# Performance work log

Measured on AMD Instinct MI355X. Metric: run time of the kernel, lower is better.

The kernel has to match this reference:

```python
import jax, jax.numpy as jnp
import numpy as np

N_HEADS = 4

def layernorm(x, g, b):
    m = jnp.mean(x, -1, keepdims=True)
    v = jnp.var(x, -1, keepdims=True)
    return (x - m) / jnp.sqrt(v + 1e-5) * g + b

def conv1d(x, w, b, pad):
    y = jax.lax.conv_general_dilated(x, w, (1,), [(pad, pad)], dimension_numbers=('NCH', 'OIH', 'NCH'))
    return y + b[None, :, None]

def bn_eval(x, g, b, m, v):
    return (x - m[None, :, None]) / jnp.sqrt(v[None, :, None] + 1e-5) * g[None, :, None] + b[None, :, None]

def maxpool(x, k):
    return jax.lax.reduce_window(x, -jnp.inf, jax.lax.max, (1, 1, k), (1, 1, k), 'VALID')

def _forward(x, conv1_w, conv1_b, bn1_g, bn1_b, bn1_m, bn1_v, conv2_w, conv2_b, bn2_g, bn2_b, bn2_m, bn2_v, adj_prior, log_weights, gat_n1_g, gat_n1_b, gat_qkv_w, gat_qkv_b, gat_out_w, gat_out_b, gat_n2_g, gat_n2_b, gat_f1_w, gat_f1_b, gat_f2_w, gat_f2_b, gatn_g, gatn_b, gru_wih, gru_whh, gru_bih, gru_bhh, gate_w, gate_b):
    B, C, T = x.shape
    D = conv2_w.shape[0]
    dk = D // N_HEADS
    scale = dk ** -0.5
    # --- per-channel temporal CNN: (B,C,T) -> (B,C,T',D), T' = T//16 ---
    h = x.reshape(B * C, 1, T)
    h = maxpool(jax.nn.gelu(bn_eval(conv1d(h, conv1_w, conv1_b, 3), bn1_g, bn1_b, bn1_m, bn1_v), approximate=False), 4)
    h = maxpool(jax.nn.gelu(bn_eval(conv1d(h, conv2_w, conv2_b, 2), bn2_g, bn2_b, bn2_m, bn2_v), approximate=False), 4)
    Tp = h.shape[-1]
    h = jnp.transpose(h, (0, 2, 1)).reshape(B, C, Tp, D)
    # --- spectral dynamic adjacency ---
    h_avg = h.mean(axis=2)                                   # (B,C,D)
    hc = h_avg - h_avg.mean(-1, keepdims=True)
    hn = hc / (jnp.linalg.norm(hc, axis=-1, keepdims=True) + 1e-8)
    feat_corr = jnp.einsum('bcd,bed->bce', hn, hn)
    Xp = jnp.abs(jnp.fft.rfft(x, axis=-1))
    Xn = Xp / (jnp.linalg.norm(Xp, axis=-1, keepdims=True) + 1e-8)
    spec_coh = jnp.einsum('bcf,bef->bce', Xn, Xn)
    prior = (adj_prior + adj_prior.T)[None]
    w = jax.nn.softmax(log_weights)
    adj = w[0] * feat_corr + w[1] * spec_coh + w[2] * prior  # (B,C,C)
    # --- GAT stack over the C-node channel graph at every timestep ---
    ht = jnp.transpose(h, (0, 2, 1, 3)).reshape(B * Tp, C, D)
    adj_t = jnp.broadcast_to(adj[:, None], (B, Tp, C, C)).reshape(B * Tp, C, C)
    L = gat_qkv_w.shape[0]
    for l in range(L):
        hn1 = layernorm(ht, gat_n1_g[l], gat_n1_b[l])
        qkv = (hn1 @ gat_qkv_w[l].T + gat_qkv_b[l]).reshape(B * Tp, C, 3, N_HEADS, dk)
        q = jnp.moveaxis(qkv[:, :, 0], 1, 2)                 # (N,H,C,dk)
        k = jnp.moveaxis(qkv[:, :, 1], 1, 2)
        v = jnp.moveaxis(qkv[:, :, 2], 1, 2)
        attn = jnp.einsum('nhqd,nhkd->nhqk', q, k) * scale + adj_t[:, None]
        attn = jax.nn.softmax(attn, axis=-1)                 # dropout off (eval)
        out = jnp.einsum('nhqk,nhkd->nhqd', attn, v)
        out = jnp.moveaxis(out, 1, 2).reshape(B * Tp, C, D)
        ht = ht + out @ gat_out_w[l].T + gat_out_b[l]
        hn2 = layernorm(ht, gat_n2_g[l], gat_n2_b[l])
        ffn = jax.nn.gelu(hn2 @ gat_f1_w[l].T + gat_f1_b[l], approximate=False) @ gat_f2_w[l].T + gat_f2_b[l]
        ht = ht + ffn
    ht = layernorm(ht, gatn_g, gatn_b)
    hs = ht.reshape(B, Tp, C, D).transpose(0, 2, 1, 3).reshape(B * C, Tp, D)
    # --- bidirectional GRU (1 layer), final hidden states only ---
    G = gru_whh.shape[-1]
    def gru_last(xs, wih, whh, bih, bhh):
        def step(hprev, xt):
            gi = xt @ wih.T + bih
            gh = hprev @ whh.T + bhh
            ir, iz, inn = jnp.split(gi, 3, -1)
            hr, hz, hnn = jnp.split(gh, 3, -1)
            r = jax.nn.sigmoid(ir + hr)
            z = jax.nn.sigmoid(iz + hz)
            n = jnp.tanh(inn + r * hnn)
            hnew = (1.0 - z) * n + z * hprev
            return hnew, None
        h0 = jnp.zeros((xs.shape[0], G), xs.dtype)
        hl, _ = jax.lax.scan(step, h0, jnp.moveaxis(xs, 1, 0))
        return hl
    h_f = gru_last(hs, gru_wih[0], gru_whh[0], gru_bih[0], gru_bhh[0])
    h_b = gru_last(hs[:, ::-1], gru_wih[1], gru_whh[1], gru_bih[1], gru_bhh[1])
    h_out = jnp.concatenate([h_f, h_b], -1).reshape(B, C, 2 * G)
    # --- channel-attention readout ---
    gate = jax.nn.sigmoid(h_out @ gate_w.T + gate_b)         # (B,C,1)
    readout = (h_out * gate).sum(1) / (gate.sum(1) + 1e-8)   # (B,2G)
    return readout, adj, gate

def setup_inputs() -> dict:
    key = jax.random.key(0)
    ks = iter(jax.random.split(key, 64))
    B, C, T = 32, 16, 4096
    D, L, G = 64, 2, 64
    def rn(shape, s=0.08):
        return jax.random.normal(next(ks), shape, jnp.float32) * s
    return dict(
        x=jax.random.normal(next(ks), (B, C, T), jnp.float32),
        conv1_w=rn((32, 1, 7), 0.2), conv1_b=rn((32,)),
        bn1_g=jnp.ones((32,)), bn1_b=jnp.zeros((32,)), bn1_m=jnp.zeros((32,)), bn1_v=jnp.ones((32,)),
        conv2_w=rn((D, 32, 5), 0.1), conv2_b=rn((D,)),
        bn2_g=jnp.ones((D,)), bn2_b=jnp.zeros((D,)), bn2_m=jnp.zeros((D,)), bn2_v=jnp.ones((D,)),
        adj_prior=rn((C, C), 0.1), log_weights=jnp.zeros((3,)),
        gat_n1_g=jnp.ones((L, D)), gat_n1_b=jnp.zeros((L, D)),
        gat_qkv_w=rn((L, 3 * D, D)), gat_qkv_b=jnp.zeros((L, 3 * D)),
        gat_out_w=rn((L, D, D)), gat_out_b=jnp.zeros((L, D)),
        gat_n2_g=jnp.ones((L, D)), gat_n2_b=jnp.zeros((L, D)),
        gat_f1_w=rn((L, 2 * D, D)), gat_f1_b=jnp.zeros((L, 2 * D)),
        gat_f2_w=rn((L, D, 2 * D)), gat_f2_b=jnp.zeros((L, D)),
        gatn_g=jnp.ones((D,)), gatn_b=jnp.zeros((D,)),
        gru_wih=rn((2, 3 * G, D)), gru_whh=rn((2, 3 * G, G)),
        gru_bih=jnp.zeros((2, 3 * G)), gru_bhh=jnp.zeros((2, 3 * G)),
        gate_w=rn((1, 2 * G)), gate_b=jnp.zeros((1,)),
    )

def reference(x, conv1_w, conv1_b, bn1_g, bn1_b, bn1_m, bn1_v, conv2_w, conv2_b, bn2_g, bn2_b, bn2_m, bn2_v, adj_prior, log_weights, gat_n1_g, gat_n1_b, gat_qkv_w, gat_qkv_b, gat_out_w, gat_out_b, gat_n2_g, gat_n2_b, gat_f1_w, gat_f1_b, gat_f2_w, gat_f2_b, gatn_g, gatn_b, gru_wih, gru_whh, gru_bih, gru_bhh, gate_w, gate_b):
    return _forward(x, conv1_w, conv1_b, bn1_g, bn1_b, bn1_m, bn1_v, conv2_w, conv2_b, bn2_g, bn2_b, bn2_m, bn2_v, adj_prior, log_weights, gat_n1_g, gat_n1_b, gat_qkv_w, gat_qkv_b, gat_out_w, gat_out_b, gat_n2_g, gat_n2_b, gat_f1_w, gat_f1_b, gat_f2_w, gat_f2_b, gatn_g, gatn_b, gru_wih, gru_whh, gru_bih, gru_bhh, gate_w, gate_b)
```

## Files before the change

### kernel.cpp

```cpp
#include <hip/hip_runtime.h>
#include <hip/hip_bf16.h>
#include <math.h>

typedef __hip_bfloat16 bf16;
typedef unsigned short ushort_t;
typedef __attribute__((ext_vector_type(8))) short short8;
typedef __attribute__((ext_vector_type(4))) float f32x4;

__device__ __forceinline__ float b2f(bf16 v) { return __bfloat162float(v); }
__device__ __forceinline__ bf16 f2b(float v) { return __float2bfloat16(v); }
__device__ __forceinline__ float bflo(unsigned u) { return __uint_as_float(u << 16); }
__device__ __forceinline__ float bfhi(unsigned u) { return __uint_as_float(u & 0xffff0000u); }
__device__ __forceinline__ float sigmoidf_(float x) { return 1.0f / (1.0f + __expf(-x)); }

__device__ __forceinline__ float geluf(float x) {
    float z = x * 0.70710678118654752f;
    float az = fabsf(z);
    float t = 1.0f / (1.0f + 0.3275911f * az);
    float poly = ((((1.061405429f * t - 1.453152027f) * t + 1.421413741f) * t
                   - 0.284496736f) * t + 0.254829592f) * t;
    float erfa = 1.0f - poly * __expf(-z * z);
    float er = (z < 0.f) ? -erfa : erfa;
    return 0.5f * x * (1.0f + er);
}

__device__ __forceinline__ unsigned pack2bf(float a, float b) {
    unsigned ua = __float_as_uint(a); ua = (ua + 0x7FFFu + ((ua >> 16) & 1u)) >> 16;
    unsigned ub = __float_as_uint(b); ub = (ub + 0x7FFFu + ((ub >> 16) & 1u)) >> 16;
    return ua | (ub << 16);
}
__device__ __forceinline__ ushort_t f2bu(float v) {
    unsigned u = __float_as_uint(v);
    u = (u + 0x7FFFu + ((u >> 16) & 1u)) >> 16;
    return (ushort_t)u;
}

__global__ __launch_bounds__(256) void k_detect(const unsigned* __restrict__ x, int* __restrict__ flag)
{
    __shared__ int cnt;
    if (threadIdx.x == 0) cnt = 0;
    __syncthreads();
    unsigned u = x[threadIdx.x] & 0xFFFFu;
    float f = __uint_as_float(u << 16);
    float a = fabsf(f);
    int sane = (f == 0.0f) || (a > 1e-8f && a < 1e4f);
    atomicAdd(&cnt, sane);
    __syncthreads();
    if (threadIdx.x == 0) *flag = (cnt >= 160) ? 1 : 0;
}

struct InPtrs { const void* p[35]; };
struct InOffs { int off[35]; int sz[35]; };

__global__ __launch_bounds__(256) void k_convert(InPtrs P, InOffs O, int total,
                                                 const int* __restrict__ flag,
                                                 float* __restrict__ cvt)
{
    int idx = blockIdx.x * 256 + threadIdx.x;
    if (idx >= total) return;
    int isb = *flag;
    float v = 0.f;
#pragma unroll 1
    for (int s = 0; s < 35; s++) {
        int rel = idx - O.off[s];
        if (rel >= 0 && rel < O.sz[s]) {
            v = isb ? b2f(((const bf16*)P.p[s])[rel]) : ((const float*)P.p[s])[rel];
            break;
        }
    }
    cvt[idx] = v;
}

__global__ __launch_bounds__(256) void k_pack(const float* __restrict__ qw, const float* __restrict__ ow,
                                              const float* __restrict__ f1w, const float* __restrict__ f2w,
                                              const float* __restrict__ gwih, const float* __restrict__ gwhh,
                                              const float* __restrict__ c2w,
                                              unsigned* __restrict__ dst)
{
    int i = blockIdx.x * 256 + threadIdx.x;
    if (i >= 62464) return;
    if (i >= 57344) {
        int j0 = (i - 57344) * 2;
        int tap = j0 >> 11, rem = j0 & 2047;
        int d = rem >> 5, ic = rem & 31;
        dst[i] = pack2bf(c2w[d * 160 + ic * 5 + tap], c2w[d * 160 + (ic + 1) * 5 + tap]);
        return;
    }
    const float* s; int rel;
    if (i < 12288)      { s = qw;   rel = i; }
    else if (i < 16384) { s = ow;   rel = i - 12288; }
    else if (i < 24576) { s = f1w;  rel = i - 16384; }
    else if (i < 32768) { s = f2w;  rel = i - 24576; }
    else if (i < 45056) { s = gwih; rel = i - 32768; }
    else                { s = gwhh; rel = i - 45056; }
    dst[i] = pack2bf(s[2 * rel], s[2 * rel + 1]);
}

__global__ __launch_bounds__(256) void k_cnn(
    const float* __restrict__ x, const float* __restrict__ c1w, const float* __restrict__ c1b,
    const float* __restrict__ bn1g, const float* __restrict__ bn1b, const float* __restrict__ bn1m, const float* __restrict__ bn1v,
    const float* __restrict__ c2b,
    const float* __restrict__ bn2g, const float* __restrict__ bn2b, const float* __restrict__ bn2m, const float* __restrict__ bn2v,
    const ushort_t* __restrict__ w2pk,
    float* __restrict__ h_main)
{
    __shared__ float ubuf[4352];
    __shared__ ushort_t h1t[260 * 40];
    __shared__ float A2s[64], B2s[64];
    int bc = blockIdx.x, t = threadIdx.x;
    int l = t & 63, w = t >> 6;
    int lo = l & 15, quad = l >> 4;

    if (t < 64) {
        float s = bn2g[t] * rsqrtf(bn2v[t] + 1e-5f);
        A2s[t] = s; B2s[t] = (c2b[t] - bn2m[t]) * s + bn2b[t];
    }
    int icp = t & 15;
    float w1r[2][7], A1r[2], B1r[2];
#pragma unroll
    for (int s = 0; s < 2; s++) {
        int ic = icp * 2 + s;
#pragma unroll
        for (int k = 0; k < 7; k++) w1r[s][k] = c1w[ic * 7 + k];
        float sc = bn1g[ic] * rsqrtf(bn1v[ic] + 1e-5f);
        A1r[s] = sc; B1r[s] = (c1b[ic] - bn1m[ic]) * sc + bn1b[ic];
    }
    short8 Afr[4][5];
#pragma unroll
    for (int dt = 0; dt < 4; dt++)
#pragma unroll
        for (int tap = 0; tap < 5; tap++)
            Afr[dt][tap] = *(const short8*)(w2pk + ((tap * 64 + dt * 16 + lo) * 32 + quad * 8));

    const float* xrow = x + (size_t)bc * 4096;
    for (int tile = 0; tile < 4; tile++) {
        int X0 = 1024 * tile - 11;
        for (int i = t; i < 1056; i += 256) {
            int g = X0 + i;
            ubuf[i] = (g >= 0 && g < 4096) ? xrow[g] : 0.0f;
        }
        __syncthreads();
        for (int pos = (t >> 4); pos < 260; pos += 16) {
            const float4* xw = (const float4*)&ubuf[4 * pos];
            float4 fa = xw[0], fb = xw[1], fc = xw[2];
            float xv[12] = {fa.x, fa.y, fa.z, fa.w, fb.x, fb.y, fb.z, fb.w,
                            fc.x, fc.y, fc.z, fc.w};
            int t1pg = tile * 256 + pos - 2;
            bool ok = (t1pg >= 0 && t1pg < 1024);
            float res[2];
#pragma unroll
            for (int s = 0; s < 2; s++) {
                float a0 = 0.f, a1 = 0.f, a2 = 0.f, a3 = 0.f;
#pragma unroll
                for (int k = 0; k < 7; k++) {
                    float wv = w1r[s][k];
                    a0 += xv[k] * wv;     a1 += xv[k + 1] * wv;
                    a2 += xv[k + 2] * wv; a3 += xv[k + 3] * wv;
                }
                float A = A1r[s], B = B1r[s];
                a0 = a0 * A + B; a1 = a1 * A + B; a2 = a2 * A + B; a3 = a3 * A + B;
                float mx = fmaxf(fmaxf(a0, a1), fmaxf(a2, a3));
                float mn = fminf(fminf(a0, a1), fminf(a2, a3));
                res[s] = ok ? fmaxf(geluf(mx), geluf(mn)) : 0.0f;
            }
            ((unsigned*)h1t)[pos * 20 + icp] = pack2bf(res[0], res[1]);
        }
        __syncthreads();
        float* houtile = ubuf;
#pragma unroll
        for (int ni = 0; ni < 4; ni++) {
            int nt = w * 4 + ni;
            short8 bf[5];
#pragma unroll
            for (int tap = 0; tap < 5; tap++)
                bf[tap] = *(const short8*)&h1t[(nt * 16 + lo + tap) * 40 + quad * 8];
#pragma unroll
            for (int dt = 0; dt < 4; dt++) {
                f32x4 acc = {0.f, 0.f, 0.f, 0.f};
#pragma unroll
                for (int tap = 0; tap < 5; tap++)
                    acc = __builtin_amdgcn_mfma_f32_16x16x32_bf16(Afr[dt][tap], bf[tap], acc, 0, 0, 0);
                const float4 a2 = *(const float4*)&A2s[dt * 16 + quad * 4];
                const float4 b2 = *(const float4*)&B2s[dt * 16 + quad * 4];
                float a2a[4] = {a2.x, a2.y, a2.z, a2.w};
                float b2a[4] = {b2.x, b2.y, b2.z, b2.w};
#pragma unroll
                for (int r = 0; r < 4; r++) {
                    float v = acc[r] * a2a[r] + b2a[r];
                    float o1 = __shfl_xor(v, 1);
                    float mx = fmaxf(v, o1), mn = fminf(v, o1);
                    float mx2 = __shfl_xor(mx, 2), mn2 = __shfl_xor(mn, 2);
                    mx = fmaxf(mx, mx2); mn = fminf(mn, mn2);
                    float res = fmaxf(geluf(mx), geluf(mn));
                    if ((lo & 3) == 0)
                        houtile[(nt * 4 + (lo >> 2)) * 68 + dt * 16 + quad * 4 + r] = res;
                }
            }
        }
        __syncthreads();
        float* dst = h_main + (size_t)bc * 16384 + tile * 4096;
        for (int i = t * 4; i < 4096; i += 1024) {
            float4 v = *(const float4*)&ubuf[(i >> 6) * 68 + (i & 63)];
            *(float4*)&dst[i] = v;
        }
        __syncthreads();
    }
}

__global__ __launch_bounds__(512) void k_fft(const float* __restrict__ x, float* __restrict__ Xn)
{
    __shared__ float re[4096];
    __shared__ float im[4096];
    __shared__ float red[8];
    int bc = blockIdx.x, t = threadIdx.x;
    const float* xr = x + (size_t)bc * 4096;
    for (int i = t; i < 4096; i += 512) {
        int r = __brev((unsigned)i) >> 20;
        re[r] = xr[i];
        im[r] = 0.f;
    }
    __syncthreads();
    for (int s = 1; s <= 12; s++) {
        int half = 1 << (s - 1);
        float ang = -6.283185307179586f / (float)(1 << s);
        for (int m = t; m < 2048; m += 512) {
            int j = m & (half - 1);
            int pos = ((m >> (s - 1)) << s) | j;
            float sn, cs;
            __sincosf(ang * (float)j, &sn, &cs);
            float ur = re[pos], ui = im[pos];
            float vr = re[pos + half], vi = im[pos + half];
            float tr = vr * cs - vi * sn;
            float ti = vr * sn + vi * cs;
            re[pos] = ur + tr; im[pos] = ui + ti;
            re[pos + half] = ur - tr; im[pos + half] = ui - ti;
        }
        __syncthreads();
    }
    float mag[5];
    float ss = 0.f;
    int cnt = 0;
    for (int f = t; f <= 2048; f += 512) {
        float m2 = re[f] * re[f] + im[f] * im[f];
        mag[cnt++] = sqrtf(m2);
        ss += m2;
    }
    for (int off = 32; off; off >>= 1) ss += __shfl_xor(ss, off, 64);
    if ((t & 63) == 0) red[t >> 6] = ss;
    __syncthreads();
    float tot = 0.f;
#pragma unroll
    for (int i = 0; i < 8; i++) tot += red[i];
    float inv = 1.0f / (sqrtf(tot) + 1e-8f);
    cnt = 0;
    for (int f = t; f <= 2048; f += 512) Xn[(size_t)bc * 2049 + f] = mag[cnt++] * inv;
}

__global__ __launch_bounds__(64) void k_havg(const float* __restrict__ hm, float* __restrict__ hnf)
{
    int bc = blockIdx.x, d = threadIdx.x;
    const float* base = hm + (size_t)bc * 16384;
    float s = 0.f;
    for (int tp = 0; tp < 256; tp++) s += base[tp * 64 + d];
    float avg = s * (1.0f / 256.0f);
    float tot = avg;
    for (int off = 32; off; off >>= 1) tot += __shfl_xor(tot, off, 64);
    float hc = avg - tot * (1.0f / 64.0f);
    float sq = hc * hc;
    for (int off = 32; off; off >>= 1) sq += __shfl_xor(sq, off, 64);
    hnf[bc * 64 + d] = hc / (sqrtf(sq) + 1e-8f);
}

__global__ __launch_bounds__(256) void k_adj(
    const float* __restrict__ Xn, const float* __restrict__ hnf,
    const float* __restrict__ prior, const float* __restrict__ logw,
    float* __restrict__ adjw, void* __restrict__ out, const int* __restrict__ flag)
{
    __shared__ float xt[16][257];
    __shared__ float hh[16 * 64];
    int b = blockIdx.x, t = threadIdx.x;
    int c = t >> 4, e = t & 15;
    for (int i = t; i < 1024; i += 256) hh[i] = hnf[b * 1024 + i];
    __syncthreads();
    float fc = 0.f;
    for (int d = 0; d < 64; d++) fc += hh[c * 64 + d] * hh[e * 64 + d];
    float sc = 0.f;
    const float* Xb = Xn + (size_t)b * 16 * 2049;
    for (int f0 = 0; f0 < 2048; f0 += 256) {
        __syncthreads();
        for (int i = t; i < 16 * 256; i += 256) {
            int rr = i >> 8, ff = i & 255;
            xt[rr][ff] = Xb[rr * 2049 + f0 + ff];
        }
        __syncthreads();
        for (int ff = 0; ff < 256; ff++) sc += xt[c][ff] * xt[e][ff];
    }
    sc += Xb[c * 2049 + 2048] * Xb[e * 2049 + 2048];
    float l0 = logw[0], l1 = logw[1], l2 = logw[2];
    float mx = fmaxf(l0, fmaxf(l1, l2));
    float e0 = __expf(l0 - mx), e1 = __expf(l1 - mx), e2 = __expf(l2 - mx);
    float isum = 1.0f / (e0 + e1 + e2);
    float pr = prior[c * 16 + e] + prior[e * 16 + c];
    float v = (e0 * fc + e1 * sc + e2 * pr) * isum;
    adjw[b * 256 + t] = v;
    if (*flag) ((bf16*)out)[4096 + b * 256 + t] = f2b(v);
    else       ((float*)out)[4096 + b * 256 + t] = v;
}

__device__ __forceinline__ void ln_wave(const float (*ht)[68], ushort_t (*out)[72],
                                        const float* __restrict__ g, const float* __restrict__ bp,
                                        int quad, int lo)
{
    float v[16];
    const float4* row = (const float4*)(&ht[lo][quad * 16]);
#pragma unroll
    for (int i = 0; i < 4; i++) {
        float4 a = row[i];
        v[4 * i] = a.x; v[4 * i + 1] = a.y; v[4 * i + 2] = a.z; v[4 * i + 3] = a.w;
    }
    float s = 0.f;
#pragma unroll
    for (int i = 0; i < 16; i++) s += v[i];
    s += __shfl_xor(s, 16); s += __shfl_xor(s, 32);
    float mean = s * (1.0f / 64.0f);
    float q = 0.f;
#pragma unroll
    for (int i = 0; i < 16; i++) { float d = v[i] - mean; q += d * d; }
    q += __shfl_xor(q, 16); q += __shfl_xor(q, 32);
    float rstd = rsqrtf(q * (1.0f / 64.0f) + 1e-5f);
    const float4* gp = (const float4*)(g + quad * 16);
    const float4* bb4 = (const float4*)(bp + quad * 16);
    unsigned* orow = (unsigned*)(&out[lo][quad * 16]);
#pragma unroll
    for (int i = 0; i < 4; i++) {
        float4 gg = gp[i], bb = bb4[i];
        float o0 = (v[4 * i] - mean) * rstd * gg.x + bb.x;
        float o1 = (v[4 * i + 1] - mean) * rstd * gg.y + bb.y;
        float o2 = (v[4 * i + 2] - mean) * rstd * gg.z + bb.z;
        float o3 = (v[4 * i + 3] - mean) * rstd * gg.w + bb.w;
        orow[2 * i] = pack2bf(o0, o1);
        orow[2 * i + 1] = pack2bf(o2, o3);
    }
}

__global__ __launch_bounds__(256) void k_gat(
    const float* __restrict__ hm, const float* __restrict__ adjw,
    const ushort_t* __restrict__ wpk,
    const float* __restrict__ qb_, const float* __restrict__ ob_,
    const float* __restrict__ f1b_, const float* __restrict__ f2b_,
    const float* __restrict__ n1g_, const float* __restrict__ n1b_,
    const float* __restrict__ n2g_, const float* __restrict__ n2b_,
    const float* __restrict__ gng, const float* __restrict__ gnb,
    ushort_t* __restrict__ hmb)
{
    __shared__ float htw_all[4][16][68];
    __shared__ ushort_t hnw_all[4][16][72];
    __shared__ ushort_t qkb_all[4][16][200];
    __shared__ ushort_t pb_all[4][16][72];
    __shared__ ushort_t vt_all[4][64][24];
    int t = threadIdx.x;
    int w = t >> 6, l = t & 63;
    int quad = l >> 4, lo = l & 15;
    int n = blockIdx.x * 4 + w;
    int b = n >> 8, tp = n & 255;
    float (*htw)[68] = htw_all[w];
    ushort_t (*hnw)[72] = hnw_all[w];
    ushort_t (*qkb)[200] = qkb_all[w];
    ushort_t (*pb)[72] = pb_all[w];
    ushort_t (*vt)[24] = vt_all[w];
    const float* src = hm + (size_t)b * 16 * 16384 + (size_t)tp * 64;
#pragma unroll
    for (int c = 0; c < 16; c++) htw[c][l] = src[(size_t)c * 16384 + l];
    float adjr[4];
#pragma unroll
    for (int r = 0; r < 4; r++) adjr[r] = adjw[b * 256 + (quad * 4 + r) * 16 + lo];

    for (int layer = 0; layer < 2; layer++) {
        const ushort_t* wq  = wpk + layer * 12288;
        const ushort_t* wo  = wpk + 24576 + layer * 4096;
        const ushort_t* wf1 = wpk + 32768 + layer * 8192;
        const ushort_t* wf2 = wpk + 49152 + layer * 8192;
        const float* qb = qb_ + layer * 192;
        const float* ob = ob_ + layer * 64;
        const float* f1b = f1b_ + layer * 128;
        const float* f2b = f2b_ + layer * 64;

        ln_wave(htw, hnw, n1g_ + layer * 64, n1b_ + layer * 64, quad, lo);

        short8 a0 = *(const short8*)&hnw[lo][quad * 8];
        short8 a1 = *(const short8*)&hnw[lo][32 + quad * 8];
#pragma unroll
        for (int nt = 0; nt < 12; nt++) {
            const ushort_t* wr = wq + (nt * 16 + lo) * 64 + quad * 8;
            short8 b0 = *(const short8*)wr;
            short8 b1 = *(const short8*)(wr + 32);
            f32x4 acc = {0.f, 0.f, 0.f, 0.f};
            acc = __builtin_amdgcn_mfma_f32_16x16x32_bf16(a0, b0, acc, 0, 0, 0);
            acc = __builtin_amdgcn_mfma_f32_16x16x32_bf16(a1, b1, acc, 0, 0, 0);
            float bias = qb[nt * 16 + lo];
            if (nt < 8) {
#pragma unroll
                for (int r = 0; r < 4; r++) qkb[quad * 4 + r][nt * 16 + lo] = f2bu(acc[r] + bias);
            } else {
#pragma unroll
                for (int r = 0; r < 4; r++) vt[(nt - 8) * 16 + lo][quad * 4 + r] = f2bu(acc[r] + bias);
            }
        }

        short8 zf = {0, 0, 0, 0, 0, 0, 0, 0};
#pragma unroll
        for (int h = 0; h < 4; h++) {
            short8 qf = zf, kf = zf;
            if (quad < 2) {
                qf = *(const short8*)&qkb[lo][h * 16 + quad * 8];
                kf = *(const short8*)&qkb[lo][64 + h * 16 + quad * 8];
            }
            f32x4 s4 = {0.f, 0.f, 0.f, 0.f};
            s4 = __builtin_amdgcn_mfma_f32_16x16x32_bf16(qf, kf, s4, 0, 0, 0);
#pragma unroll
            for (int r = 0; r < 4; r++) {
                float sv = s4[r] * 0.25f + adjr[r];
                float mx = sv;
                mx = fmaxf(mx, __shfl_xor(mx, 1));
                mx = fmaxf(mx, __shfl_xor(mx, 2));
                mx = fmaxf(mx, __shfl_xor(mx, 4));
                mx = fmaxf(mx, __shfl_xor(mx, 8));
                float e = __expf(sv - mx);
                float sm = e;
                sm += __shfl_xor(sm, 1);
                sm += __shfl_xor(sm, 2);
                sm += __shfl_xor(sm, 4);
                sm += __shfl_xor(sm, 8);
                pb[quad * 4 + r][h * 16 + lo] = f2bu(e / sm);
            }
        }
#pragma unroll
        for (int h = 0; h < 4; h++) {
            short8 pf = zf, vf = zf;
            if (quad < 2) {
                pf = *(const short8*)&pb[lo][h * 16 + quad * 8];
                vf = *(const short8*)&vt[h * 16 + lo][quad * 8];
            }
            f32x4 oc = {0.f, 0.f, 0.f, 0.f};
            oc = __builtin_amdgcn_mfma_f32_16x16x32_bf16(pf, vf, oc, 0, 0, 0);
#pragma unroll
            for (int r = 0; r < 4; r++) qkb[quad * 4 + r][h * 16 + lo] = f2bu(oc[r]);
        }
        short8 pa0 = *(const short8*)&qkb[lo][quad * 8];
        short8 pa1 = *(const short8*)&qkb[lo][32 + quad * 8];
#pragma unroll
        for (int nt = 0; nt < 4; nt++) {
            const ushort_t* wr = wo + (nt * 16 + lo) * 64 + quad * 8;
            short8 b0 = *(const short8*)wr;
            short8 b1 = *(const short8*)(wr + 32);
            f32x4 acc = {0.f, 0.f, 0.f, 0.f};
            acc = __builtin_amdgcn_mfma_f32_16x16x32_bf16(pa0, b0, acc, 0, 0, 0);
            acc = __builtin_amdgcn_mfma_f32_16x16x32_bf16(pa1, b1, acc, 0, 0, 0);
            float bias = ob[nt * 16 + lo];
#pragma unroll
            for (int r = 0; r < 4; r++) htw[quad * 4 + r][nt * 16 + lo] += acc[r] + bias;
        }
        ln_wave(htw, hnw, n2g_ + layer * 64, n2b_ + layer * 64, quad, lo);
        short8 fa0 = *(const short8*)&hnw[lo][quad * 8];
        short8 fa1 = *(const short8*)&hnw[lo][32 + quad * 8];
#pragma unroll
        for (int nt = 0; nt < 8; nt++) {
            const ushort_t* wr = wf1 + (nt * 16 + lo) * 64 + quad * 8;
            short8 b0 = *(const short8*)wr;
            short8 b1 = *(const short8*)(wr + 32);
            f32x4 acc = {0.f, 0.f, 0.f, 0.f};
            acc = __builtin_amdgcn_mfma_f32_16x16x32_bf16(fa0, b0, acc, 0, 0, 0);
            acc = __builtin_amdgcn_mfma_f32_16x16x32_bf16(fa1, b1, acc, 0, 0, 0);
            float bias = f1b[nt * 16 + lo];
#pragma unroll
            for (int r = 0; r < 4; r++) qkb[quad * 4 + r][nt * 16 + lo] = f2bu(geluf(acc[r] + bias));
        }
        short8 ga[4];
#pragma unroll
        for (int kb = 0; kb < 4; kb++) ga[kb] = *(const short8*)&qkb[lo][kb * 32 + quad * 8];
#pragma unroll
        for (int nt = 0; nt < 4; nt++) {
            const ushort_t* wr = wf2 + (nt * 16 + lo) * 128 + quad * 8;
            f32x4 acc = {0.f, 0.f, 0.f, 0.f};
#pragma unroll
            for (int kb = 0; kb < 4; kb++) {
                short8 bb = *(const short8*)(wr + kb * 32);
                acc = __builtin_amdgcn_mfma_f32_16x16x32_bf16(ga[kb], bb, acc, 0, 0, 0);
            }
            float bias = f2b[nt * 16 + lo];
#pragma unroll
            for (int r = 0; r < 4; r++) htw[quad * 4 + r][nt * 16 + lo] += acc[r] + bias;
        }
    }
    {
        float v[16];
        const float4* row = (const float4*)(&htw[lo][quad * 16]);
#pragma unroll
        for (int i = 0; i < 4; i++) {
            float4 a = row[i];
            v[4 * i] = a.x; v[4 * i + 1] = a.y; v[4 * i + 2] = a.z; v[4 * i + 3] = a.w;
        }
        float s = 0.f;
#pragma unroll
        for (int i = 0; i < 16; i++) s += v[i];
        s += __shfl_xor(s, 16); s += __shfl_xor(s, 32);
        float mean = s * (1.0f / 64.0f);
        float q = 0.f;
#pragma unroll
        for (int i = 0; i < 16; i++) { float d = v[i] - mean; q += d * d; }
        q += __shfl_xor(q, 16); q += __shfl_xor(q, 32);
        float rstd = rsqrtf(q * (1.0f / 64.0f) + 1e-5f);
        const float4* gp = (const float4*)(gng + quad * 16);
        const float4* bb4 = (const float4*)(gnb + quad * 16);
        unsigned u[8];
#pragma unroll
        for (int i = 0; i < 4; i++) {
            float4 gg = gp[i], bb = bb4[i];
            float o0 = (v[4 * i] - mean) * rstd * gg.x + bb.x;
            float o1 = (v[4 * i + 1] - mean) * rstd * gg.y + bb.y;
            float o2 = (v[4 * i + 2] - mean) * rstd * gg.z + bb.z;
            float o3 = (v[4 * i + 3] - mean) * rstd * gg.w + bb.w;
            u[2 * i] = pack2bf(o0, o1);
            u[2 * i + 1] = pack2bf(o2, o3);
        }
        ushort_t* dst = hmb + (size_t)(b * 16 + lo) * 16384 + (size_t)tp * 64 + quad * 16;
        ((uint4*)dst)[0] = make_uint4(u[0], u[1], u[2], u[3]);
        ((uint4*)dst)[1] = make_uint4(u[4], u[5], u[6], u[7]);
    }
}

__global__ __launch_bounds__(256) void k_gru(
    const ushort_t* __restrict__ hmb, const ushort_t* __restrict__ wgru,
    const float* __restrict__ bih_, const float* __restrict__ bhh_,
    float* __restrict__ h_out)
{
    __shared__ ushort_t hbuf[2][16][72];
    int t = threadIdx.x;
    int w = t >> 6, l = t & 63;
    int ln = l & 15, qd = l >> 4;
    int dir = blockIdx.x >> 5;
    int cseq0 = (blockIdx.x & 31) * 16;
    const ushort_t* wih = wgru + dir * 12288;
    const ushort_t* whh = wgru + 24576 + dir * 12288;
    const ushort_t* pr0 = wih + ((w)*16 + ln) * 64 + qd * 8;
    const ushort_t* pz0 = wih + ((4 + w)*16 + ln) * 64 + qd * 8;
    const ushort_t* pn0 = wih + ((8 + w)*16 + ln) * 64 + qd * 8;
    const ushort_t* hr0 = whh + ((w)*16 + ln) * 64 + qd * 8;
    const ushort_t* hz0 = whh + ((4 + w)*16 + ln) * 64 + qd * 8;
    const ushort_t* hn0 = whh + ((8 + w)*16 + ln) * 64 + qd * 8;
    short8 wi_r0 = *(const short8*)pr0, wi_r1 = *(const short8*)(pr0 + 32);
    short8 wi_z0 = *(const short8*)pz0, wi_z1 = *(const short8*)(pz0 + 32);
    short8 wi_n0 = *(const short8*)pn0, wi_n1 = *(const short8*)(pn0 + 32);
    short8 wh_r0 = *(const short8*)hr0, wh_r1 = *(const short8*)(hr0 + 32);
    short8 wh_z0 = *(const short8*)hz0, wh_z1 = *(const short8*)(hz0 + 32);
    short8 wh_n0 = *(const short8*)hn0, wh_n1 = *(const short8*)(hn0 + 32);
    int d = w * 16 + ln;
    float bs_r = bih_[dir * 192 + d] + bhh_[dir * 192 + d];
    float bs_z = bih_[dir * 192 + 64 + d] + bhh_[dir * 192 + 64 + d];
    float bi_n = bih_[dir * 192 + 128 + d];
    float bh_n = bhh_[dir * 192 + 128 + d];
    const ushort_t* xrow = hmb + (size_t)(cseq0 + ln) * 16384 + qd * 8;
    for (int i = t; i < 2 * 16 * 72; i += 256) ((ushort_t*)hbuf)[i] = 0;
    float h_old[4] = {0.f, 0.f, 0.f, 0.f};
    int tt0 = dir ? 255 : 0;
    short8 xc0 = *(const short8*)(xrow + tt0 * 64);
    short8 xc1 = *(const short8*)(xrow + tt0 * 64 + 32);
    __syncthreads();
#pragma unroll 2
    for (int step = 0; step < 256; step++) {
        int cur = step & 1, nxt = cur ^ 1;
        short8 ah0 = *(const short8*)&hbuf[cur][ln][qd * 8];
        short8 ah1 = *(const short8*)&hbuf[cur][ln][32 + qd * 8];
        f32x4 ar = {0.f, 0.f, 0.f, 0.f}, az = {0.f, 0.f, 0.f, 0.f};
        f32x4 ani = {0.f, 0.f, 0.f, 0.f}, anh = {0.f, 0.f, 0.f, 0.f};
        ar = __builtin_amdgcn_mfma_f32_16x16x32_bf16(xc0, wi_r0, ar, 0, 0, 0);
        ar = __builtin_amdgcn_mfma_f32_16x16x32_bf16(xc1, wi_r1, ar, 0, 0, 0);
        ar = __builtin_amdgcn_mfma_f32_16x16x32_bf16(ah0, wh_r0, ar, 0, 0, 0);
        ar = __builtin_amdgcn_mfma_f32_16x16x32_bf16(ah1, wh_r1, ar, 0, 0, 0);
        az = __builtin_amdgcn_mfma_f32_16x16x32_bf16(xc0, wi_z0, az, 0, 0, 0);
        az = __builtin_amdgcn_mfma_f32_16x16x32_bf16(xc1, wi_z1, az, 0, 0, 0);
        az = __builtin_amdgcn_mfma_f32_16x16x32_bf16(ah0, wh_z0, az, 0, 0, 0);
        az = __builtin_amdgcn_mfma_f32_16x16x32_bf16(ah1, wh_z1, az, 0, 0, 0);
        ani = __builtin_amdgcn_mfma_f32_16x16x32_bf16(xc0, wi_n0, ani, 0, 0, 0);
        ani = __builtin_amdgcn_mfma_f32_16x16x32_bf16(xc1, wi_n1, ani, 0, 0, 0);
        anh = __builtin_amdgcn_mfma_f32_16x16x32_bf16(ah0, wh_n0, anh, 0, 0, 0);
        anh = __builtin_amdgcn_mfma_f32_16x16x32_bf16(ah1, wh_n1, anh, 0, 0, 0);
        if (step < 255) {
            int tn = dir ? (254 - step) : (step + 1);
            xc0 = *(const short8*)(xrow + tn * 64);
            xc1 = *(const short8*)(xrow + tn * 64 + 32);
        }
#pragma unroll
        for (int r = 0; r < 4; r++) {
            float gr = sigmoidf_(ar[r] + bs_r);
            float gz = sigmoidf_(az[r] + bs_z);
            float nin = (ani[r] + bi_n) + gr * (anh[r] + bh_n);
            nin = fminf(fmaxf(nin, -15.f), 15.f);
            float e = __expf(-2.f * nin);
            float gn = (1.f - e) / (1.f + e);
            float hn = gn + gz * (h_old[r] - gn);
            h_old[r] = hn;
            hbuf[nxt][qd * 4 + r][d] = f2bu(hn);
        }
        __syncthreads();
    }
#pragma unroll
    for (int r = 0; r < 4; r++)
        h_out[(size_t)(cseq0 + qd * 4 + r) * 128 + dir * 64 + d] = h_old[r];
}

__global__ __launch_bounds__(128) void k_readout(
    const float* __restrict__ h_out, const float* __restrict__ gw, const float* __restrict__ gb,
    void* __restrict__ out, const int* __restrict__ flag)
{
    __shared__ float gate_s[16];
    __shared__ float gws[128];
    int b = blockIdx.x, t = threadIdx.x;
    gws[t] = gw[t];
    __syncthreads();
    int isb = *flag;
    if (t < 16) {
        const float* hr = h_out + (size_t)(b * 16 + t) * 128;
        float acc = gb[0];
        for (int k = 0; k < 128; k++) acc += hr[k] * gws[k];
        float g = sigmoidf_(acc);
        gate_s[t] = g;
        if (isb) ((bf16*)out)[12288 + b * 16 + t] = f2b(g);
        else     ((float*)out)[12288 + b * 16 + t] = g;
    }
    __syncthreads();
    float den = 1e-8f;
#pragma unroll
    for (int c = 0; c < 16; c++) den += gate_s[c];
    float num = 0.f;
#pragma unroll
    for (int c = 0; c < 16; c++) num += h_out[(size_t)(b * 16 + c) * 128 + t] * gate_s[c];
    float v = num / den;
    if (isb) ((bf16*)out)[b * 128 + t] = f2b(v);
    else     ((float*)out)[b * 128 + t] = v;
}

extern "C" void kernel_launch(void* const* d_in, const int* in_sizes, int n_in,
                              void* d_out, int out_size, void* d_ws, size_t ws_size,
                              hipStream_t stream)
{
    int* flag = (int*)d_ws;
    float* cvt = (float*)((char*)d_ws + 256);

    InPtrs P;
    InOffs O;
    int cum = 0;
    for (int i = 0; i < 35; i++) {
        P.p[i] = d_in[i];
        O.off[i] = cum;
        O.sz[i] = in_sizes[i];
        cum += (in_sizes[i] + 7) & ~7;
    }
    int total = cum;

    const float* x     = cvt + O.off[0];
    const float* c1w   = cvt + O.off[1];
    const float* c1b   = cvt + O.off[2];
    const float* bn1g  = cvt + O.off[3];
    const float* bn1b  = cvt + O.off[4];
    const float* bn1m  = cvt + O.off[5];
    const float* bn1v  = cvt + O.off[6];
    const float* c2w   = cvt + O.off[7];
    const float* c2b   = cvt + O.off[8];
    const float* bn2g  = cvt + O.off[9];
    const float* bn2b  = cvt + O.off[10];
    const float* bn2m  = cvt + O.off[11];
    const float* bn2v  = cvt + O.off[12];
    const float* prior = cvt + O.off[13];
    const float* logw  = cvt + O.off[14];
    const float* n1g   = cvt + O.off[15];
    const float* n1b   = cvt + O.off[16];
    const float* qkvw  = cvt + O.off[17];
    const float* qkvb  = cvt + O.off[18];
    const float* outw  = cvt + O.off[19];
    const float* outb  = cvt + O.off[20];
    const float* n2g   = cvt + O.off[21];
    const float* n2b   = cvt + O.off[22];
    const float* f1w   = cvt + O.off[23];
    const float* f1b   = cvt + O.off[24];
    const float* f2w   = cvt + O.off[25];
    const float* f2b_  = cvt + O.off[26];
    const float* gng   = cvt + O.off[27];
    const float* gnb   = cvt + O.off[28];
    const float* gwih  = cvt + O.off[29];
    const float* gwhh  = cvt + O.off[30];
    const float* gbih  = cvt + O.off[31];
    const float* gbhh  = cvt + O.off[32];
    const float* gatew = cvt + O.off[33];
    const float* gateb = cvt + O.off[34];

    float* fbase = cvt + ((total + 63) & ~63);
    float* hm   = fbase;
    float* Xn   = hm + 8388608;
    float* hnf  = Xn + 1049088;
    float* adjw = hnf + 32768;
    float* hout = adjw + 8192;
    unsigned* wpk = (unsigned*)(hout + 65536);
    ushort_t* hmb = (ushort_t*)(wpk + 62464);

    k_detect<<<1, 256, 0, stream>>>((const unsigned*)d_in[0], flag);
    k_convert<<<(total + 255) / 256, 256, 0, stream>>>(P, O, total, flag, cvt);
    k_pack<<<244, 256, 0, stream>>>(qkvw, outw, f1w, f2w, gwih, gwhh, c2w, wpk);
    k_cnn<<<512, 256, 0, stream>>>(x, c1w, c1b, bn1g, bn1b, bn1m, bn1v,
                                   c2b, bn2g, bn2b, bn2m, bn2v,
                                   (const ushort_t*)(wpk + 57344), hm);
    k_fft<<<512, 512, 0, stream>>>(x, Xn);
    k_havg<<<512, 64, 0, stream>>>(hm, hnf);
    k_adj<<<32, 256, 0, stream>>>(Xn, hnf, prior, logw, adjw, d_out, flag);
    k_gat<<<2048, 256, 0, stream>>>(hm, adjw, (const ushort_t*)wpk,
                                    qkvb, outb, f1b, f2b_, n1g, n1b, n2g, n2b, gng, gnb, hmb);
    k_gru<<<64, 256, 0, stream>>>(hmb, (const ushort_t*)(wpk + 32768), gbih, gbhh, hout);
    k_readout<<<32, 128, 0, stream>>>(hout, gatew, gateb, d_out, flag);
}
```

Before: 678.8 us.

## Software-pipeline GRU input projection one step ahead and prefetch inputs two steps ahead

The GRU recurrence loop now computes the input-to-hidden MFMA products for the next timestep while the current step's hidden-state products run, and loads x rows two steps ahead. Only the hidden-state MFMAs stay on the serial dependency chain, which shortens the per-step critical path. The __syncthreads is also replaced by an inline s_waitcnt lgkmcnt(0) plus s_barrier, which skips the vmcnt wait so the global prefetch loads can stay in flight across the barrier. In exchange the code uses more registers for the extra accumulators and buffered inputs, and it depends on hand-written barrier semantics.

```diff
diff --git a/kernel.cpp b/kernel.cpp
--- a/kernel.cpp
+++ b/kernel.cpp
@@ -562,39 +562,54 @@
     const ushort_t* xrow = hmb + (size_t)(cseq0 + ln) * 16384 + qd * 8;
     for (int i = t; i < 2 * 16 * 72; i += 256) ((ushort_t*)hbuf)[i] = 0;
     float h_old[4] = {0.f, 0.f, 0.f, 0.f};
-    int tt0 = dir ? 255 : 0;
-    short8 xc0 = *(const short8*)(xrow + tt0 * 64);
-    short8 xc1 = *(const short8*)(xrow + tt0 * 64 + 32);
+
+    int s0 = dir ? 255 : 0;
+    int s1 = dir ? 254 : 1;
+    int s2 = dir ? 253 : 2;
+    short8 xc0 = *(const short8*)(xrow + s0 * 64);
+    short8 xc1 = *(const short8*)(xrow + s0 * 64 + 32);
+    short8 xA0 = *(const short8*)(xrow + s1 * 64);
+    short8 xA1 = *(const short8*)(xrow + s1 * 64 + 32);
+    short8 xB0 = *(const short8*)(xrow + s2 * 64);
+    short8 xB1 = *(const short8*)(xrow + s2 * 64 + 32);
+    f32x4 axr = {0.f, 0.f, 0.f, 0.f}, axz = {0.f, 0.f, 0.f, 0.f}, axn = {0.f, 0.f, 0.f, 0.f};
+    axr = __builtin_amdgcn_mfma_f32_16x16x32_bf16(xc0, wi_r0, axr, 0, 0, 0);
+    axr = __builtin_amdgcn_mfma_f32_16x16x32_bf16(xc1, wi_r1, axr, 0, 0, 0);
+    axz = __builtin_amdgcn_mfma_f32_16x16x32_bf16(xc0, wi_z0, axz, 0, 0, 0);
+    axz = __builtin_amdgcn_mfma_f32_16x16x32_bf16(xc1, wi_z1, axz, 0, 0, 0);
+    axn = __builtin_amdgcn_mfma_f32_16x16x32_bf16(xc0, wi_n0, axn, 0, 0, 0);
+    axn = __builtin_amdgcn_mfma_f32_16x16x32_bf16(xc1, wi_n1, axn, 0, 0, 0);
     __syncthreads();
 #pragma unroll 2
     for (int step = 0; step < 256; step++) {
         int cur = step & 1, nxt = cur ^ 1;
+        f32x4 nxr = {0.f, 0.f, 0.f, 0.f}, nxz = {0.f, 0.f, 0.f, 0.f}, nxn = {0.f, 0.f, 0.f, 0.f};
+        nxr = __builtin_amdgcn_mfma_f32_16x16x32_bf16(xA0, wi_r0, nxr, 0, 0, 0);
+        nxr = __builtin_amdgcn_mfma_f32_16x16x32_bf16(xA1, wi_r1, nxr, 0, 0, 0);
+        nxz = __builtin_amdgcn_mfma_f32_16x16x32_bf16(xA0, wi_z0, nxz, 0, 0, 0);
+        nxz = __builtin_amdgcn_mfma_f32_16x16x32_bf16(xA1, wi_z1, nxz, 0, 0, 0);
+        nxn = __builtin_amdgcn_mfma_f32_16x16x32_bf16(xA0, wi_n0, nxn, 0, 0, 0);
+        nxn = __builtin_amdgcn_mfma_f32_16x16x32_bf16(xA1, wi_n1, nxn, 0, 0, 0);
+        xA0 = xB0; xA1 = xB1;
+        int tl = step + 3 > 255 ? 255 : step + 3;
+        int sf = dir ? 255 - tl : tl;
+        xB0 = *(const short8*)(xrow + sf * 64);
+        xB1 = *(const short8*)(xrow + sf * 64 + 32);
         short8 ah0 = *(const short8*)&hbuf[cur][ln][qd * 8];
         short8 ah1 = *(const short8*)&hbuf[cur][ln][32 + qd * 8];
-        f32x4 ar = {0.f, 0.f, 0.f, 0.f}, az = {0.f, 0.f, 0.f, 0.f};
-        f32x4 ani = {0.f, 0.f, 0.f, 0.f}, anh = {0.f, 0.f, 0.f, 0.f};
-        ar = __builtin_amdgcn_mfma_f32_16x16x32_bf16(xc0, wi_r0, ar, 0, 0, 0);
-        ar = __builtin_amdgcn_mfma_f32_16x16x32_bf16(xc1, wi_r1, ar, 0, 0, 0);
+        f32x4 ar = axr, az = axz;
+        f32x4 anh = {0.f, 0.f, 0.f, 0.f};
         ar = __builtin_amdgcn_mfma_f32_16x16x32_bf16(ah0, wh_r0, ar, 0, 0, 0);
         ar = __builtin_amdgcn_mfma_f32_16x16x32_bf16(ah1, wh_r1, ar, 0, 0, 0);
-        az = __builtin_amdgcn_mfma_f32_16x16x32_bf16(xc0, wi_z0, az, 0, 0, 0);
-        az = __builtin_amdgcn_mfma_f32_16x16x32_bf16(xc1, wi_z1, az, 0, 0, 0);
         az = __builtin_amdgcn_mfma_f32_16x16x32_bf16(ah0, wh_z0, az, 0, 0, 0);
         az = __builtin_amdgcn_mfma_f32_16x16x32_bf16(ah1, wh_z1, az, 0, 0, 0);
-        ani = __builtin_amdgcn_mfma_f32_16x16x32_bf16(xc0, wi_n0, ani, 0, 0, 0);
-        ani = __builtin_amdgcn_mfma_f32_16x16x32_bf16(xc1, wi_n1, ani, 0, 0, 0);
         anh = __builtin_amdgcn_mfma_f32_16x16x32_bf16(ah0, wh_n0, anh, 0, 0, 0);
         anh = __builtin_amdgcn_mfma_f32_16x16x32_bf16(ah1, wh_n1, anh, 0, 0, 0);
-        if (step < 255) {
-            int tn = dir ? (254 - step) : (step + 1);
-            xc0 = *(const short8*)(xrow + tn * 64);
-            xc1 = *(const short8*)(xrow + tn * 64 + 32);
-        }
 #pragma unroll
         for (int r = 0; r < 4; r++) {
             float gr = sigmoidf_(ar[r] + bs_r);
             float gz = sigmoidf_(az[r] + bs_z);
-            float nin = (ani[r] + bi_n) + gr * (anh[r] + bh_n);
+            float nin = (axn[r] + bi_n) + gr * (anh[r] + bh_n);
             nin = fminf(fmaxf(nin, -15.f), 15.f);
             float e = __expf(-2.f * nin);
             float gn = (1.f - e) / (1.f + e);
@@ -602,7 +617,8 @@
             h_old[r] = hn;
             hbuf[nxt][qd * 4 + r][d] = f2bu(hn);
         }
-        __syncthreads();
+        asm volatile("s_waitcnt lgkmcnt(0)\n\ts_barrier" ::: "memory");
+        axr = nxr; axz = nxz; axn = nxn;
     }
 #pragma unroll
     for (int r = 0; r < 4; r++)
```

Result: no change. 669.8 us (-1.3%).
